# Performance work log

Hardware: AMD Instinct MI355X
Metric: run time of the kernel (lower is better)

## Reference

```python
import jax, jax.numpy as jnp
import numpy as np


def conv2d(x, w, pad, groups=1):
    # x: [B,Cin,H,W], w: [Cout,Cin/groups,K,K]
    return jax.lax.conv_general_dilated(
        x, w, (1, 1), [(pad, pad), (pad, pad)],
        dimension_numbers=('NCHW', 'OIHW', 'NCHW'),
        feature_group_count=groups)


def setup_inputs() -> dict:
    key = jax.random.key(0)
    ks = jax.random.split(key, 24)
    B, C, H, W = 16, 512, 32, 128          # batch, encoder_dim, feature map
    Da, Ds, De, Dm = 512, 256, 256, 1024   # att_dim, state_dim, embed_dim, mem_dim
    V, Dmerge = 1000, 512
    K, P = 11, 5
    Din = De + C + Dm                       # GRU input dim = 1792
    s = 0.02
    rn = lambda k, shp, sc=1.0: jax.random.normal(k, shp, jnp.float32) * sc
    return {
        'encode': rn(ks[0], (B, C, H, W)),
        'encode_pro': rn(ks[1], (B, Da, H, W)),
        'encode_mask': jnp.ones((B, 1, H, W), jnp.float32),
        'state': rn(ks[2], (B, Ds)),
        'pre_weight': jax.random.uniform(ks[3], (B, 1, H, W), jnp.float32),
        'cum_weight': jax.random.uniform(ks[4], (B, 1, H, W), jnp.float32),
        'context': rn(ks[5], (B, C)),
        'cond_mem': rn(ks[6], (B, Dm)),
        'cond_weight': jax.random.uniform(ks[7], (B, 2, H, W), jnp.float32),
        'label_id': jax.random.randint(ks[8], (B,), 0, V),
        # ImageAttention params (all bias-free per source)
        'w_wt': rn(ks[9], (Da, 1, K, K), s),
        'w_cwt': rn(ks[10], (Da, 1, K, K), s),
        'w_condwt': rn(ks[11], (2 * Da, 1, K, K), s),   # groups=2
        'w_energy': rn(ks[12], (Da,), s),               # 1x1 conv -> vector
        'w_state': rn(ks[13], (Da, Ds), s),
        'w_ctx': rn(ks[14], (Da, C), s),
        'w_cond': rn(ks[15], (Da, Dm), s),
        # GRU params
        'w_i2s': rn(ks[16], (Ds, Din), s), 'b_i2s': jnp.zeros((Ds,), jnp.float32),
        'w_i2g': rn(ks[17], (2 * Ds, Din), s), 'b_i2g': jnp.zeros((2 * Ds,), jnp.float32),
        'w_s2g': rn(ks[18], (2 * Ds, Ds), s),
        'w_h2h': rn(ks[19], (Ds, Ds), s),
        # Readout params
        'embed_table': rn(ks[20], (V, De), s),
        'w_l1': rn(ks[21], (Dmerge, De + Ds + C), s), 'b_l1': jnp.zeros((Dmerge,), jnp.float32),
        'w_l2': rn(ks[22], (V, Dmerge), s), 'b_l2': jnp.zeros((V,), jnp.float32),
    }


def reference(encode, encode_pro, encode_mask, state, pre_weight, cum_weight,
              context, cond_mem, cond_weight, label_id, w_wt, w_cwt, w_condwt,
              w_energy, w_state, w_ctx, w_cond, w_i2s, b_i2s, w_i2g, b_i2g,
              w_s2g, w_h2h, embed_table, w_l1, b_l1, w_l2, b_l2):
    P = (w_wt.shape[-1] - 1) // 2
    Da = w_energy.shape[0]
    B, C, H, W = encode.shape
    # --- ImageAttention ---
    t_pre = conv2d(pre_weight, w_wt, P)           # [B,Da,H,W]
    t_cum = conv2d(cum_weight, w_cwt, P)          # [B,Da,H,W]
    t_cw = conv2d(cond_weight, w_condwt, P, groups=2)
    t_cw = t_cw.reshape(B, 2, Da, H, W).sum(1)    # [B,Da,H,W]
    st = state @ w_state.T + context @ w_ctx.T + cond_mem @ w_cond.T  # [B,Da]
    concat_info = jnp.tanh(st[:, :, None, None] + t_pre + t_cum + t_cw + encode_pro)
    energies = jnp.einsum('bchw,c->bhw', concat_info, w_energy)
    energies = energies + (encode_mask[:, 0] - 1.0) * 1e8
    att = jax.nn.softmax(energies.reshape(B, H * W), axis=1)
    new_weight = att.reshape(B, 1, H, W)
    new_cum_weight = cum_weight + new_weight
    ctx = jnp.einsum('bchw,bhw->bc', encode, new_weight[:, 0])  # [B,C]
    # --- GRU transition (data = [embed, ctx, cond_mem]) ---
    embed = embed_table[label_id]
    data = jnp.concatenate([embed, ctx, cond_mem], axis=1)
    gate = data @ w_i2g.T + b_i2g + state @ w_s2g.T
    Ds = state.shape[1]
    update_g = jax.nn.sigmoid(gate[:, :Ds])
    reset_g = jax.nn.sigmoid(gate[:, Ds:])
    state_hat = jnp.tanh(data @ w_i2s.T + b_i2s + (state * reset_g) @ w_h2h.T)
    new_state = update_g * state_hat + (1.0 - update_g) * state
    # --- Readout.step ---
    merged = jnp.concatenate([embed, new_state, ctx], axis=1)
    hid = jax.nn.relu(merged @ w_l1.T + b_l1)
    readout = hid @ w_l2.T + b_l2                  # [B,V]
    return readout
```

## Files before the change

kernel.cpp:

```cpp
#include <hip/hip_runtime.h>
#include <math.h>

typedef unsigned short u16;
typedef __bf16 bf16x8 __attribute__((ext_vector_type(8)));
typedef float f32x4 __attribute__((ext_vector_type(4)));

__device__ u16   g_A_pack[16 * 512 * 32];
__device__ float g_st[16 * 512];
__device__ float g_eraw[16 * 4096];
__device__ float g_energ[16 * 4096];
__device__ float g_data[16 * 1792];
__device__ float g_merged[16 * 1024];
__device__ float g_update[16 * 256];
__device__ float g_reset[16 * 256];
__device__ float g_i2s[16 * 256];
__device__ float g_hid[16 * 512];

__device__ __forceinline__ u16 f2bf(float f) {
    unsigned u = __float_as_uint(f);
    u = (u + 0x7FFFu + ((u >> 16) & 1u)) >> 16;
    return (u16)u;
}
__device__ __forceinline__ float bf2f(u16 u) {
    return __uint_as_float(((unsigned)u) << 16);
}
__device__ __forceinline__ float fast_tanh(float x) {
    return 1.0f - 2.0f / (__expf(2.0f * x) + 1.0f);
}
__device__ __forceinline__ float sigmoidf_(float x) {
    return 1.0f / (1.0f + __expf(-x));
}

__global__ void k_prep(const float* __restrict__ w_wt, const float* __restrict__ w_cwt,
                       const float* __restrict__ w_condwt) {
    int idx = blockIdx.x * blockDim.x + threadIdx.x;
    if (idx >= 512 * 512) return;
    int d = idx >> 9, k = idx & 511;
    float f = 0.f;
    if (k < 484) {
        int c = k / 121, rem = k % 121;
        if (c == 0)      f = w_wt[d * 121 + rem];
        else if (c == 1) f = w_cwt[d * 121 + rem];
        else if (c == 2) f = w_condwt[d * 121 + rem];
        else             f = w_condwt[(512 + d) * 121 + rem];
    }
    int ks = k >> 5, kl = k & 31;
    g_A_pack[(ks * 512 + d) * 32 + kl] = f2bf(f);
}

__global__ void k_st(const float* __restrict__ state, const float* __restrict__ context,
                     const float* __restrict__ cond_mem, const float* __restrict__ w_state,
                     const float* __restrict__ w_ctx, const float* __restrict__ w_cond) {
    int wid = (blockIdx.x * blockDim.x + threadIdx.x) >> 6;
    int lane = threadIdx.x & 63;
    if (wid >= 16 * 512) return;
    int b = wid >> 9, d = wid & 511;
    float acc = 0.f;
    for (int k = lane; k < 256; k += 64)  acc += state[b * 256 + k]    * w_state[d * 256 + k];
    for (int k = lane; k < 512; k += 64)  acc += context[b * 512 + k]  * w_ctx[d * 512 + k];
    for (int k = lane; k < 1024; k += 64) acc += cond_mem[b * 1024 + k] * w_cond[d * 1024 + k];
    for (int off = 32; off; off >>= 1) acc += __shfl_down(acc, off, 64);
    if (lane == 0) g_st[b * 512 + d] = acc;
}

__global__ void k_e0(const int* __restrict__ label, const float* __restrict__ embed_table,
                     const float* __restrict__ cond_mem) {
    int b = blockIdx.x, tid = threadIdx.x;
    int lbl = label[b];
    if (tid < 256) {
        float ev = embed_table[lbl * 256 + tid];
        g_data[b * 1792 + tid] = ev;
        g_merged[b * 1024 + tid] = ev;
    }
    for (int k = tid; k < 1024; k += 256)
        g_data[b * 1792 + 768 + k] = cond_mem[b * 1024 + k];
}

__global__ __launch_bounds__(512, 4) void k_conv_energy(
    const float* __restrict__ pre_w, const float* __restrict__ cum_w, const float* __restrict__ cond_w,
    const float* __restrict__ encode_pro, const float* __restrict__ w_energy)
{
    __shared__ __align__(16) u16 src[4][11][76];
    __shared__ __align__(16) u16 bchunk[64][40];
    __shared__ __align__(16) u16 epro_l[512 * 68];

    const int blk = blockIdx.x;
    const int pxh = blk & 1;
    const int h = (blk >> 1) & 31;
    const int b = blk >> 6;
    const int px0 = pxh * 64;

    const int tid = threadIdx.x;
    const int lane = tid & 63, wv = tid >> 6;
    const int lr = lane & 15, lg = lane >> 4;

    {
        const float* epbase = encode_pro + (size_t)b * 512 * 4096 + h * 128 + px0;
#pragma unroll
        for (int i = 0; i < 16; ++i) {
            int o = i * 2048 + tid * 4;
            int r = o >> 6, c = o & 63;
            float4 v = *reinterpret_cast<const float4*>(&epbase[(size_t)r * 4096 + c]);
            ushort4 s;
            s.x = f2bf(v.x); s.y = f2bf(v.y); s.z = f2bf(v.z); s.w = f2bf(v.w);
            *reinterpret_cast<ushort4*>(&epro_l[r * 68 + c]) = s;
        }
    }

#pragma unroll
    for (int it = 0; it < 7; ++it) {
        int t = tid + it * 512;
        if (t < 4 * 11 * 76) {
            int c = t / (11 * 76);
            int rem = t % (11 * 76);
            int i = rem / 76, x = rem % 76;
            int row = h + i - 5, w = px0 - 5 + x;
            u16 v = 0;
            if (x < 74 && row >= 0 && row < 32 && w >= 0 && w < 128) {
                const float* img = (c == 0) ? pre_w + b * 4096
                                 : (c == 1) ? cum_w + b * 4096
                                 : (c == 2) ? cond_w + b * 8192
                                            : cond_w + b * 8192 + 4096;
                v = f2bf(img[row * 128 + w]);
            }
            src[c][i][x] = v;
        }
    }
    __syncthreads();

    const int kl = tid & 31;
    const int n0 = tid >> 5;
#define BUILD(KS)                                                               \
    {                                                                           \
        int kg = (KS) * 32 + kl;                                                \
        int c = 0, i = 0, jj = 0;                                               \
        bool ok = (kg < 484);                                                   \
        if (ok) { c = kg / 121; int r2 = kg % 121; i = r2 / 11; jj = r2 % 11; } \
        _Pragma("unroll")                                                       \
        for (int rep = 0; rep < 4; ++rep) {                                     \
            int n = n0 + rep * 16;                                              \
            bchunk[n][kl] = ok ? src[c][i][n + jj] : (u16)0;                    \
        }                                                                       \
    }

    f32x4 acc[4][4];
#pragma unroll
    for (int mt = 0; mt < 4; ++mt)
#pragma unroll
        for (int nt = 0; nt < 4; ++nt) {
            f32x4 z = {0.f, 0.f, 0.f, 0.f};
            acc[mt][nt] = z;
        }

    BUILD(0);
    __syncthreads();

    for (int ks = 0; ks < 16; ++ks) {
        bf16x8 afr[4];
#pragma unroll
        for (int mt = 0; mt < 4; ++mt) {
            int d = wv * 64 + mt * 16 + lr;
            afr[mt] = *reinterpret_cast<const bf16x8*>(&g_A_pack[(ks * 512 + d) * 32 + lg * 8]);
        }
        bf16x8 bfr[4];
#pragma unroll
        for (int nt = 0; nt < 4; ++nt)
            bfr[nt] = *reinterpret_cast<const bf16x8*>(&bchunk[nt * 16 + lr][lg * 8]);

#pragma unroll
        for (int mt = 0; mt < 4; ++mt)
#pragma unroll
            for (int nt = 0; nt < 4; ++nt)
                acc[mt][nt] = __builtin_amdgcn_mfma_f32_16x16x32_bf16(afr[mt], bfr[nt], acc[mt][nt], 0, 0, 0);
        __syncthreads();
        if (ks < 15) {
            BUILD(ks + 1);
            __syncthreads();
        }
    }
#undef BUILD

    float e[4] = {0.f, 0.f, 0.f, 0.f};
#pragma unroll
    for (int mt = 0; mt < 4; ++mt) {
#pragma unroll
        for (int r = 0; r < 4; ++r) {
            int d = wv * 64 + mt * 16 + lg * 4 + r;
            float stv = g_st[b * 512 + d];
            float wev = w_energy[d];
#pragma unroll
            for (int nt = 0; nt < 4; ++nt) {
                int px = nt * 16 + lr;
                float val = stv + acc[mt][nt][r] + bf2f(epro_l[d * 68 + px]);
                e[nt] += wev * fast_tanh(val);
            }
        }
    }

    float* ered = reinterpret_cast<float*>(&bchunk[0][0]);
    __syncthreads();
#pragma unroll
    for (int nt = 0; nt < 4; ++nt) {
        float v = e[nt];
        v += __shfl_xor(v, 16, 64);
        v += __shfl_xor(v, 32, 64);
        if (lane < 16) ered[wv * 64 + nt * 16 + lane] = v;
    }
    __syncthreads();
    if (tid < 64) {
        float v = 0.f;
#pragma unroll
        for (int w = 0; w < 8; ++w) v += ered[w * 64 + tid];
        g_eraw[b * 4096 + h * 128 + px0 + tid] = v;
    }
}

__global__ void k_softmax(const float* __restrict__ encode_mask) {
    __shared__ float red[256];
    int b = blockIdx.x, tid = threadIdx.x;
    float v[16];
    float mx = -1e30f;
#pragma unroll
    for (int i = 0; i < 16; ++i) {
        int idx = b * 4096 + tid + i * 256;
        float ev = g_eraw[idx] + (encode_mask[idx] - 1.0f) * 1e8f;
        v[i] = ev; mx = fmaxf(mx, ev);
    }
    red[tid] = mx; __syncthreads();
    for (int s = 128; s; s >>= 1) { if (tid < s) red[tid] = fmaxf(red[tid], red[tid + s]); __syncthreads(); }
    mx = red[0]; __syncthreads();
    float sum = 0.f;
#pragma unroll
    for (int i = 0; i < 16; ++i) { v[i] = __expf(v[i] - mx); sum += v[i]; }
    red[tid] = sum; __syncthreads();
    for (int s = 128; s; s >>= 1) { if (tid < s) red[tid] += red[tid + s]; __syncthreads(); }
    float inv = 1.0f / red[0];
#pragma unroll
    for (int i = 0; i < 16; ++i) g_energ[b * 4096 + tid + i * 256] = v[i] * inv;
}

__global__ void k_ctx(const float* __restrict__ encode) {
    int wid = (blockIdx.x * blockDim.x + threadIdx.x) >> 6;
    int lane = threadIdx.x & 63;
    if (wid >= 16 * 512) return;
    int b = wid >> 9, c = wid & 511;
    const float* e = encode + (size_t)wid * 4096;
    const float* a = g_energ + b * 4096;
    float acc = 0.f;
#pragma unroll
    for (int it = 0; it < 16; ++it) {
        int base = it * 256 + lane * 4;
        float4 ev = *reinterpret_cast<const float4*>(&e[base]);
        float4 av = *reinterpret_cast<const float4*>(&a[base]);
        acc += ev.x * av.x + ev.y * av.y + ev.z * av.z + ev.w * av.w;
    }
    for (int off = 32; off; off >>= 1) acc += __shfl_down(acc, off, 64);
    if (lane == 0) { g_data[b * 1792 + 256 + c] = acc; g_merged[b * 1024 + 512 + c] = acc; }
}

__global__ void k_e1(const float* __restrict__ state,
                     const float* __restrict__ w_i2g, const float* __restrict__ b_i2g,
                     const float* __restrict__ w_s2g, const float* __restrict__ w_i2s,
                     const float* __restrict__ b_i2s) {
    int wid = (blockIdx.x * blockDim.x + threadIdx.x) >> 6;
    int lane = threadIdx.x & 63;
    if (wid >= 16 * 768) return;
    int b = wid / 768, o = wid % 768;
    const float* dt = g_data + b * 1792;
    float acc = 0.f;
    if (o < 512) {
        const float* wr = w_i2g + o * 1792;
        for (int k = lane; k < 1792; k += 64) acc += dt[k] * wr[k];
        const float* wsg = w_s2g + o * 256;
        for (int k = lane; k < 256; k += 64) acc += state[b * 256 + k] * wsg[k];
    } else {
        const float* wr = w_i2s + (o - 512) * 1792;
        for (int k = lane; k < 1792; k += 64) acc += dt[k] * wr[k];
    }
    for (int off = 32; off; off >>= 1) acc += __shfl_down(acc, off, 64);
    if (lane == 0) {
        if (o < 256)       g_update[b * 256 + o]        = sigmoidf_(acc + b_i2g[o]);
        else if (o < 512)  g_reset[b * 256 + (o - 256)] = sigmoidf_(acc + b_i2g[o]);
        else               g_i2s[b * 256 + (o - 512)]   = acc + b_i2s[o - 512];
    }
}

__global__ void k_e2(const float* __restrict__ state, const float* __restrict__ w_h2h) {
    int wid = (blockIdx.x * blockDim.x + threadIdx.x) >> 6;
    int lane = threadIdx.x & 63;
    if (wid >= 16 * 256) return;
    int b = wid >> 8, d = wid & 255;
    const float* wr = w_h2h + d * 256;
    float acc = 0.f;
    for (int k = lane; k < 256; k += 64)
        acc += state[b * 256 + k] * g_reset[b * 256 + k] * wr[k];
    for (int off = 32; off; off >>= 1) acc += __shfl_down(acc, off, 64);
    if (lane == 0) {
        float sh = fast_tanh(g_i2s[b * 256 + d] + acc);
        float u = g_update[b * 256 + d];
        g_merged[b * 1024 + 256 + d] = u * sh + (1.f - u) * state[b * 256 + d];
    }
}

__global__ void k_e3(const float* __restrict__ w_l1, const float* __restrict__ b_l1) {
    int wid = (blockIdx.x * blockDim.x + threadIdx.x) >> 6;
    int lane = threadIdx.x & 63;
    if (wid >= 16 * 512) return;
    int b = wid >> 9, m = wid & 511;
    const float* mg = g_merged + b * 1024;
    const float* wr = w_l1 + m * 1024;
    float acc = 0.f;
    for (int k = lane; k < 1024; k += 64) acc += mg[k] * wr[k];
    for (int off = 32; off; off >>= 1) acc += __shfl_down(acc, off, 64);
    if (lane == 0) g_hid[b * 512 + m] = fmaxf(acc + b_l1[m], 0.f);
}

__global__ void k_e4(const float* __restrict__ w_l2, const float* __restrict__ b_l2,
                     float* __restrict__ out) {
    int wid = (blockIdx.x * blockDim.x + threadIdx.x) >> 6;
    int lane = threadIdx.x & 63;
    if (wid >= 16 * 1000) return;
    int b = wid / 1000, v = wid % 1000;
    const float* hd = g_hid + b * 512;
    const float* wr = w_l2 + v * 512;
    float acc = 0.f;
    for (int k = lane; k < 512; k += 64) acc += hd[k] * wr[k];
    for (int off = 32; off; off >>= 1) acc += __shfl_down(acc, off, 64);
    if (lane == 0) out[b * 1000 + v] = acc + b_l2[v];
}

extern "C" void kernel_launch(void* const* d_in, const int* in_sizes, int n_in,
                              void* d_out, int out_size, void* d_ws, size_t ws_size,
                              hipStream_t stream) {
    static const int EXP[28] = {
        33554432, 33554432, 65536, 4096, 65536, 65536, 8192, 16384, 131072, 16,
        61952, 61952, 123904, 512, 131072, 262144, 524288, 458752, 256, 917504,
        512, 131072, 65536, 256000, 524288, 512, 512000, 1000};
    if (n_in != 28) return;
    for (int i = 0; i < 28; ++i)
        if (in_sizes[i] != EXP[i]) return;

    const float* encode      = (const float*)d_in[0];
    const float* encode_pro  = (const float*)d_in[1];
    const float* encode_mask = (const float*)d_in[2];
    const float* state       = (const float*)d_in[3];
    const float* pre_weight  = (const float*)d_in[4];
    const float* cum_weight  = (const float*)d_in[5];
    const float* context     = (const float*)d_in[6];
    const float* cond_mem    = (const float*)d_in[7];
    const float* cond_weight = (const float*)d_in[8];
    const int*   label_id    = (const int*)d_in[9];
    const float* w_wt     = (const float*)d_in[10];
    const float* w_cwt    = (const float*)d_in[11];
    const float* w_condwt = (const float*)d_in[12];
    const float* w_energy = (const float*)d_in[13];
    const float* w_state  = (const float*)d_in[14];
    const float* w_ctx    = (const float*)d_in[15];
    const float* w_cond   = (const float*)d_in[16];
    const float* w_i2s    = (const float*)d_in[17];
    const float* b_i2s    = (const float*)d_in[18];
    const float* w_i2g    = (const float*)d_in[19];
    const float* b_i2g    = (const float*)d_in[20];
    const float* w_s2g    = (const float*)d_in[21];
    const float* w_h2h    = (const float*)d_in[22];
    const float* embed_t  = (const float*)d_in[23];
    const float* w_l1     = (const float*)d_in[24];
    const float* b_l1     = (const float*)d_in[25];
    const float* w_l2     = (const float*)d_in[26];
    const float* b_l2     = (const float*)d_in[27];
    float* out = (float*)d_out;
    (void)d_ws; (void)ws_size;

    k_prep<<<1024, 256, 0, stream>>>(w_wt, w_cwt, w_condwt);
    k_st<<<2048, 256, 0, stream>>>(state, context, cond_mem, w_state, w_ctx, w_cond);
    k_e0<<<16, 256, 0, stream>>>(label_id, embed_t, cond_mem);
    k_conv_energy<<<1024, 512, 0, stream>>>(pre_weight, cum_weight, cond_weight,
                                            encode_pro, w_energy);
    k_softmax<<<16, 256, 0, stream>>>(encode_mask);
    k_ctx<<<2048, 256, 0, stream>>>(encode);
    k_e1<<<3072, 256, 0, stream>>>(state, w_i2g, b_i2g, w_s2g, w_i2s, b_i2s);
    k_e2<<<1024, 256, 0, stream>>>(state, w_h2h);
    k_e3<<<2048, 256, 0, stream>>>(w_l1, b_l1);
    k_e4<<<4000, 256, 0, stream>>>(w_l2, b_l2, out);
}
```

Before: 168.4 us.

## Merge prep kernels into one launch and stream encode_pro loads through MFMA loop

The three small preparation kernels (filter packing, state projection, embedding gather) are merged into one launch that dispatches on block index, removing two kernel launches. In the conv-energy kernel, the upfront load and bf16 conversion of the encode_pro tile is replaced by a rolling 4-deep register buffer. Each K-step now converts and stores one slice into LDS and prefetches a later slice, so global loads overlap the MFMA loop. This raises register pressure under the 512-thread, 4-blocks launch bound and fully unrolls the K loop.

```diff
diff --git a/kernel.cpp b/kernel.cpp
--- a/kernel.cpp
+++ b/kernel.cpp
@@ -31,49 +31,46 @@
     return 1.0f / (1.0f + __expf(-x));
 }
 
-__global__ void k_prep(const float* __restrict__ w_wt, const float* __restrict__ w_cwt,
-                       const float* __restrict__ w_condwt) {
-    int idx = blockIdx.x * blockDim.x + threadIdx.x;
-    if (idx >= 512 * 512) return;
-    int d = idx >> 9, k = idx & 511;
-    float f = 0.f;
-    if (k < 484) {
-        int c = k / 121, rem = k % 121;
-        if (c == 0)      f = w_wt[d * 121 + rem];
-        else if (c == 1) f = w_cwt[d * 121 + rem];
-        else if (c == 2) f = w_condwt[d * 121 + rem];
-        else             f = w_condwt[(512 + d) * 121 + rem];
-    }
-    int ks = k >> 5, kl = k & 31;
-    g_A_pack[(ks * 512 + d) * 32 + kl] = f2bf(f);
-}
-
-__global__ void k_st(const float* __restrict__ state, const float* __restrict__ context,
-                     const float* __restrict__ cond_mem, const float* __restrict__ w_state,
-                     const float* __restrict__ w_ctx, const float* __restrict__ w_cond) {
-    int wid = (blockIdx.x * blockDim.x + threadIdx.x) >> 6;
-    int lane = threadIdx.x & 63;
-    if (wid >= 16 * 512) return;
-    int b = wid >> 9, d = wid & 511;
-    float acc = 0.f;
-    for (int k = lane; k < 256; k += 64)  acc += state[b * 256 + k]    * w_state[d * 256 + k];
-    for (int k = lane; k < 512; k += 64)  acc += context[b * 512 + k]  * w_ctx[d * 512 + k];
-    for (int k = lane; k < 1024; k += 64) acc += cond_mem[b * 1024 + k] * w_cond[d * 1024 + k];
-    for (int off = 32; off; off >>= 1) acc += __shfl_down(acc, off, 64);
-    if (lane == 0) g_st[b * 512 + d] = acc;
-}
-
-__global__ void k_e0(const int* __restrict__ label, const float* __restrict__ embed_table,
-                     const float* __restrict__ cond_mem) {
-    int b = blockIdx.x, tid = threadIdx.x;
-    int lbl = label[b];
-    if (tid < 256) {
+__global__ void k_pre(const float* __restrict__ w_wt, const float* __restrict__ w_cwt,
+                      const float* __restrict__ w_condwt, const float* __restrict__ state,
+                      const float* __restrict__ context, const float* __restrict__ cond_mem,
+                      const float* __restrict__ w_state, const float* __restrict__ w_ctx,
+                      const float* __restrict__ w_cond, const int* __restrict__ label,
+                      const float* __restrict__ embed_table) {
+    int bid = blockIdx.x;
+    if (bid < 1024) {
+        int idx = bid * 256 + threadIdx.x;
+        int d = idx >> 9, k = idx & 511;
+        float f = 0.f;
+        if (k < 484) {
+            int c = k / 121, rem = k % 121;
+            if (c == 0)      f = w_wt[d * 121 + rem];
+            else if (c == 1) f = w_cwt[d * 121 + rem];
+            else if (c == 2) f = w_condwt[d * 121 + rem];
+            else             f = w_condwt[(512 + d) * 121 + rem];
+        }
+        int ks = k >> 5, kl = k & 31;
+        g_A_pack[(ks * 512 + d) * 32 + kl] = f2bf(f);
+    } else if (bid < 3072) {
+        int wid = ((bid - 1024) * 256 + threadIdx.x) >> 6;
+        int lane = threadIdx.x & 63;
+        if (wid >= 16 * 512) return;
+        int b = wid >> 9, d = wid & 511;
+        float acc = 0.f;
+        for (int k = lane; k < 256; k += 64)  acc += state[b * 256 + k]    * w_state[d * 256 + k];
+        for (int k = lane; k < 512; k += 64)  acc += context[b * 512 + k]  * w_ctx[d * 512 + k];
+        for (int k = lane; k < 1024; k += 64) acc += cond_mem[b * 1024 + k] * w_cond[d * 1024 + k];
+        for (int off = 32; off; off >>= 1) acc += __shfl_down(acc, off, 64);
+        if (lane == 0) g_st[b * 512 + d] = acc;
+    } else {
+        int b = bid - 3072, tid = threadIdx.x;
+        int lbl = label[b];
         float ev = embed_table[lbl * 256 + tid];
         g_data[b * 1792 + tid] = ev;
         g_merged[b * 1024 + tid] = ev;
-    }
-    for (int k = tid; k < 1024; k += 256)
-        g_data[b * 1792 + 768 + k] = cond_mem[b * 1024 + k];
+        for (int k = tid; k < 1024; k += 256)
+            g_data[b * 1792 + 768 + k] = cond_mem[b * 1024 + k];
+    }
 }
 
 __global__ __launch_bounds__(512, 4) void k_conv_energy(
@@ -94,17 +91,14 @@
     const int lane = tid & 63, wv = tid >> 6;
     const int lr = lane & 15, lg = lane >> 4;
 
-    {
-        const float* epbase = encode_pro + (size_t)b * 512 * 4096 + h * 128 + px0;
-#pragma unroll
-        for (int i = 0; i < 16; ++i) {
-            int o = i * 2048 + tid * 4;
-            int r = o >> 6, c = o & 63;
-            float4 v = *reinterpret_cast<const float4*>(&epbase[(size_t)r * 4096 + c]);
-            ushort4 s;
-            s.x = f2bf(v.x); s.y = f2bf(v.y); s.z = f2bf(v.z); s.w = f2bf(v.w);
-            *reinterpret_cast<ushort4*>(&epro_l[r * 68 + c]) = s;
-        }
+    const float* epbase = encode_pro + (size_t)b * 512 * 4096 + h * 128 + px0;
+
+    float4 ep[4];
+#pragma unroll
+    for (int i = 0; i < 4; ++i) {
+        int o = i * 2048 + tid * 4;
+        int r = o >> 6, c = o & 63;
+        ep[i] = *reinterpret_cast<const float4*>(&epbase[(size_t)r * 4096 + c]);
     }
 
 #pragma unroll
@@ -155,7 +149,22 @@
     BUILD(0);
     __syncthreads();
 
+#pragma unroll
     for (int ks = 0; ks < 16; ++ks) {
+        {
+            int o = ks * 2048 + tid * 4;
+            int r = o >> 6, c = o & 63;
+            float4 v = ep[ks & 3];
+            ushort4 s;
+            s.x = f2bf(v.x); s.y = f2bf(v.y); s.z = f2bf(v.z); s.w = f2bf(v.w);
+            *reinterpret_cast<ushort4*>(&epro_l[r * 68 + c]) = s;
+            if (ks < 12) {
+                int o2 = (ks + 4) * 2048 + tid * 4;
+                int r2 = o2 >> 6, c2 = o2 & 63;
+                ep[ks & 3] = *reinterpret_cast<const float4*>(&epbase[(size_t)r2 * 4096 + c2]);
+            }
+        }
+
         bf16x8 afr[4];
 #pragma unroll
         for (int mt = 0; mt < 4; ++mt) {
@@ -371,9 +380,8 @@
     float* out = (float*)d_out;
     (void)d_ws; (void)ws_size;
 
-    k_prep<<<1024, 256, 0, stream>>>(w_wt, w_cwt, w_condwt);
-    k_st<<<2048, 256, 0, stream>>>(state, context, cond_mem, w_state, w_ctx, w_cond);
-    k_e0<<<16, 256, 0, stream>>>(label_id, embed_t, cond_mem);
+    k_pre<<<3088, 256, 0, stream>>>(w_wt, w_cwt, w_condwt, state, context, cond_mem,
+                                    w_state, w_ctx, w_cond, label_id, embed_t);
     k_conv_energy<<<1024, 512, 0, stream>>>(pre_weight, cum_weight, cond_weight,
                                             encode_pro, w_energy);
     k_softmax<<<16, 256, 0, stream>>>(encode_mask);
```

Measured after the change: 198.4 us. +17.8%, slower.
